# Optimization experiments

Hardware: AMD Instinct MI355X
Metric: run time of the kernel (lower is better)

Reference implementation:

```python
import jax, jax.numpy as jnp
import numpy as np

N = 50000      # nodes
E = 800000     # edges
H = 128        # num_node_hidden_channels
G = 50         # num_edge_gaussians
F = 128        # num_node_interaction_channels (= num_filters = out dim)
S = 2          # num_state_features
B = 256        # num graphs
NCONV = 2
CUTOFF = 5.0


def _ssp(x):
    # ShiftedSoftplus: softplus(x) - log(2)
    return jax.nn.softplus(x) - jnp.log(2.0).astype(x.dtype)


def _xavier(k, shape):
    fan_in = shape[-1]
    return (jax.random.normal(k, shape) / np.sqrt(fan_in)).astype(jnp.float32)


def setup_inputs() -> dict:
    key = jax.random.key(0)
    ks = jax.random.split(key, 16)
    h = jax.random.normal(ks[0], (N, H), dtype=jnp.float32)
    edge_index = jax.random.randint(ks[1], (2, E), 0, N, dtype=jnp.int64)
    edge_weight = jax.random.uniform(ks[2], (E,), dtype=jnp.float32) * CUTOFF
    edge_attr = jax.random.normal(ks[3], (E, G), dtype=jnp.float32)
    batch = jnp.sort(jax.random.randint(ks[4], (N,), 0, B, dtype=jnp.int64))
    state_attr = jax.random.normal(ks[5], (B, S), dtype=jnp.float32)
    # parameters, stacked over n_conv layers
    params = dict(
        lin1_w=_xavier(ks[6], (NCONV, H, H + S)),
        lin1_b=jnp.zeros((NCONV, H), jnp.float32),
        mlp_w1=_xavier(ks[7], (NCONV, F, G)),
        mlp_b1=jnp.zeros((NCONV, F), jnp.float32),
        mlp_w2=_xavier(ks[8], (NCONV, F, F)),
        mlp_b2=jnp.zeros((NCONV, F), jnp.float32),
        conv_lin1_w=_xavier(ks[9], (NCONV, F, H)),
        conv_lin2_w=_xavier(ks[10], (NCONV, H, F)),
        conv_lin2_b=jnp.zeros((NCONV, H), jnp.float32),
        out_w=_xavier(ks[11], (F, H)),
        out_b=jnp.zeros((F,), jnp.float32),
    )
    return dict(h=h, edge_weight=edge_weight, edge_attr=edge_attr,
                state_attr=state_attr, **params,
                edge_index=edge_index, batch=batch)


def _forward(h, edge_weight, edge_attr, state_attr,
             lin1_w, lin1_b, mlp_w1, mlp_b1, mlp_w2, mlp_b2,
             conv_lin1_w, conv_lin2_w, conv_lin2_b, out_w, out_b,
             edge_index, batch):
    src, dst = edge_index[0], edge_index[1]   # x_j gathered from src, aggregated at dst
    nB = state_attr.shape[0]
    # cosine cutoff envelope (same for all layers)
    C = 0.5 * (jnp.cos(edge_weight * (np.pi / CUTOFF)) + 1.0)   # [E]
    counts = jax.ops.segment_sum(jnp.ones((h.shape[0],), h.dtype), batch,
                                 num_segments=nB)               # [B]
    inv_counts = 1.0 / jnp.maximum(counts, 1.0)
    for i in range(NCONV):
        sa = state_attr[batch]                                  # [N,S]
        hs = jnp.concatenate([sa, h], axis=1)                   # [N,S+H]
        h2 = hs @ lin1_w[i].T + lin1_b[i]                       # [N,H]
        # edge filter MLP * cutoff
        eh = _ssp(edge_attr @ mlp_w1[i].T + mlp_b1[i]) @ mlp_w2[i].T + mlp_b2[i]
        W = eh * C[:, None]                                     # [E,F]
        # CFConv: lift -> gather-multiply -> scatter-add
        xf = h2 @ conv_lin1_w[i].T                              # [N,F]
        msg = xf[src] * W                                       # [E,F]
        agg = jax.ops.segment_sum(msg, dst, num_segments=h.shape[0])  # [N,F]
        xc = agg @ conv_lin2_w[i].T + conv_lin2_b[i]            # [N,H]
        h = h2 + _ssp(xc)                                       # residual + act
        # segment mean pooling over graphs, then global state update
        r = jax.ops.segment_sum(h, batch, num_segments=nB) * inv_counts[:, None]
        state_attr = jnp.broadcast_to(jnp.sum(r, axis=1, keepdims=True),
                                      state_attr.shape)
    return h @ out_w.T + out_b                                  # [N,F]


def reference(h, edge_weight, edge_attr, state_attr,
              lin1_w, lin1_b, mlp_w1, mlp_b1, mlp_w2, mlp_b2,
              conv_lin1_w, conv_lin2_w, conv_lin2_b, out_w, out_b,
              edge_index, batch):
    return _forward(h, edge_weight, edge_attr, state_attr,
                    lin1_w, lin1_b, mlp_w1, mlp_b1, mlp_w2, mlp_b2,
                    conv_lin1_w, conv_lin2_w, conv_lin2_b, out_w, out_b,
                    edge_index, batch)
```

## Files before the change

kernel.cpp:

```cpp
#include <hip/hip_runtime.h>

#define NN 50000
#define EE 800000
#define HH 128
#define GG 50
#define FF 128
#define SS 2
#define BB 256
#define SLOTW 8

typedef short bf16x8 __attribute__((ext_vector_type(8)));
typedef float floatx4 __attribute__((ext_vector_type(4)));

union FragU { bf16x8 v; unsigned short u[8]; unsigned int d[4]; uint4 q; };

__device__ __forceinline__ float bf2f(unsigned short u) {
    union { unsigned int i; float f; } c; c.i = ((unsigned int)u) << 16; return c.f;
}
__device__ __forceinline__ unsigned short f2bf(float f) {
    union { float f; unsigned int i; } c; c.f = f;
    unsigned int i = c.i;
    unsigned int r = (i + 0x7fffu + ((i >> 16) & 1u)) >> 16;
    return (unsigned short)r;
}
__device__ __forceinline__ float sspf(float x) {
    float l = __logf(1.f + __expf(x));
    l = (x > 20.f) ? x : l;
    return l - 0.69314718056f;
}
__device__ __forceinline__ bf16x8 f8frag(const float* p) {
    FragU f;
#pragma unroll
    for (int j = 0; j < 8; j++) f.u[j] = f2bf(p[j]);
    return f.v;
}
__device__ __forceinline__ bf16x8 load16(const unsigned short* p) {
    FragU f; f.q = *(const uint4*)p; return f.v;
}
__device__ __forceinline__ bf16x8 loaddw(const unsigned short* p) {
    FragU f; const unsigned int* pp = (const unsigned int*)p;
#pragma unroll
    for (int t = 0; t < 4; t++) f.d[t] = pp[t];
    return f.v;
}
__device__ __forceinline__ int clampi(int v, int hi) {
    v = (v < 0) ? 0 : v;
    return (v > hi) ? hi : v;
}

__global__ __launch_bounds__(256) void kConv(const float* __restrict__ s,
                                             unsigned short* __restrict__ d, int n) {
    for (int i = blockIdx.x * 256 + threadIdx.x; i < n; i += gridDim.x * 256)
        d[i] = f2bf(s[i]);
}

__global__ __launch_bounds__(256) void kConvW(const float* __restrict__ a0,
                                              const float* __restrict__ a1,
                                              const float* __restrict__ a2,
                                              const float* __restrict__ a3,
                                              const float* __restrict__ a4,
                                              const float* __restrict__ a5,
                                              unsigned short* __restrict__ d) {
    int i = blockIdx.x * 256 + threadIdx.x;
    float v;
    if (i < 12800)        v = a0[i];
    else if (i < 45568)   v = a1[i - 12800];
    else if (i < 78336)   v = a2[i - 45568];
    else if (i < 111104)  v = a3[i - 78336];
    else if (i < 144384)  v = a4[i - 111104];
    else if (i < 160768)  v = a5[i - 144384];
    else {
        int j = i - 160768;
        int k = j & 63;
        int nl = j >> 6;
        v = (k < 50) ? a0[nl * 50 + k] : 0.f;
    }
    d[i] = f2bf(v);
}

__global__ __launch_bounds__(256) void kPrep(const int* __restrict__ batch,
                                             int* __restrict__ counts,
                                             const float* __restrict__ sa_in,
                                             float* __restrict__ stateBuf) {
    int i = blockIdx.x * 256 + threadIdx.x;
    if (i < NN) atomicAdd(&counts[clampi(batch[i], BB - 1)], 1);
    if (i < BB * SS) stateBuf[i] = sa_in[i];
}

__global__ __launch_bounds__(256) void kHist(const int* __restrict__ eidx,
                                             int* __restrict__ cnt) {
    for (int e = blockIdx.x * 256 + threadIdx.x; e < EE; e += gridDim.x * 256)
        atomicAdd(&cnt[clampi(eidx[EE + e], NN - 1)], 1);
}

__global__ __launch_bounds__(1024) void kScanA(const int* __restrict__ cnt,
                                               int* __restrict__ off,
                                               int* __restrict__ blkSum) {
    __shared__ int s[1024];
    int tid = threadIdx.x;
    int g = blockIdx.x * 1024 + tid;
    int v = (g < NN) ? cnt[g] : 0;
    s[tid] = v;
    __syncthreads();
#pragma unroll
    for (int o = 1; o < 1024; o <<= 1) {
        int x = (tid >= o) ? s[tid - o] : 0;
        __syncthreads();
        s[tid] += x;
        __syncthreads();
    }
    if (g < NN) off[g] = s[tid] - v;
    if (tid == 1023) blkSum[blockIdx.x] = s[1023];
}
__global__ void kScanB(int* __restrict__ blkSum, int nb) {
    if (threadIdx.x == 0) {
        int acc = 0;
        for (int i = 0; i < nb; i++) { int t = blkSum[i]; blkSum[i] = acc; acc += t; }
    }
}
__global__ __launch_bounds__(256) void kScanC(int* __restrict__ off,
                                              const int* __restrict__ blkSum) {
    int g = blockIdx.x * 256 + threadIdx.x;
    if (g < NN) off[g] += blkSum[g >> 10];
}

__global__ __launch_bounds__(256) void kScatter(const int* __restrict__ eidx,
                                                const float* __restrict__ ew,
                                                const int* __restrict__ off,
                                                int* __restrict__ cur,
                                                int* __restrict__ pos,
                                                int* __restrict__ ePerm,
                                                int* __restrict__ dstS,
                                                int* __restrict__ srcS,
                                                float* __restrict__ cS) {
    for (int e = blockIdx.x * 256 + threadIdx.x; e < EE; e += gridDim.x * 256) {
        int d = clampi(eidx[EE + e], NN - 1);
        int p = off[d] + atomicAdd(&cur[d], 1);
        pos[e] = p;
        ePerm[p] = e;
        dstS[p] = d;
        srcS[p] = clampi(eidx[e], NN - 1);
        float w = ew[e];
        cS[p] = 0.5f * (__cosf(w * 0.62831853072f) + 1.f);
    }
}

__global__ __launch_bounds__(256) void kPermEA(const float* __restrict__ ea,
                                               const int* __restrict__ pos,
                                               unsigned short* __restrict__ eaSb) {
    int idx = blockIdx.x * 256 + threadIdx.x;
    int e = idx >> 2, part = idx & 3;
    int p = pos[e];
    const float* src = ea + (size_t)e * 50 + part * 16;
    FragU f0, f1;
#pragma unroll
    for (int j = 0; j < 8; j++) f0.u[j] = (part * 16 + j < 50) ? f2bf(src[j]) : 0;
#pragma unroll
    for (int j = 0; j < 8; j++) f1.u[j] = (part * 16 + 8 + j < 50) ? f2bf(src[8 + j]) : 0;
    uint4* d = (uint4*)(eaSb + (size_t)p * 64 + part * 16);
    d[0] = f0.q; d[1] = f1.q;
}

__global__ __launch_bounds__(256) void kA(const unsigned short* __restrict__ hb,
                                          const unsigned short* __restrict__ l1wb,
                                          const float* __restrict__ lin1w,
                                          const float* __restrict__ lin1b,
                                          const unsigned short* __restrict__ c1wb,
                                          const float* __restrict__ stateBuf,
                                          const int* __restrict__ batch,
                                          unsigned short* __restrict__ h2b,
                                          unsigned short* __restrict__ xfb) {
    __shared__ __align__(16) unsigned short P[64][136];
    int lane = threadIdx.x & 63;
    int wave = threadIdx.x >> 6;
    int m = lane & 15, q = lane >> 4;
    int rowBase = blockIdx.x * 64 + wave * 16;
    int arow = rowBase + m;
    int arowc = (arow < NN) ? arow : (NN - 1);

    floatx4 acc[8];
#pragma unroll
    for (int t = 0; t < 8; t++) acc[t] = (floatx4){0.f, 0.f, 0.f, 0.f};

#pragma unroll
    for (int k0 = 0; k0 < 128; k0 += 32) {
        bf16x8 a = load16(hb + (size_t)arowc * 128 + k0 + q * 8);
#pragma unroll
        for (int t = 0; t < 8; t++) {
            int n = t * 16 + m;
            bf16x8 b = loaddw(l1wb + (size_t)n * 130 + 2 + k0 + q * 8);
            acc[t] = __builtin_amdgcn_mfma_f32_16x16x32_bf16(a, b, acc[t], 0, 0, 0);
        }
    }

    int r0 = rowBase + q * 4;
    float s0[4], s1[4];
#pragma unroll
    for (int j = 0; j < 4; j++) {
        int r = r0 + j; int rc = (r < NN) ? r : (NN - 1);
        int g = clampi(batch[rc], BB - 1);
        s0[j] = stateBuf[g * 2 + 0];
        s1[j] = stateBuf[g * 2 + 1];
    }
#pragma unroll
    for (int t = 0; t < 8; t++) {
        int c = t * 16 + m;
        float w0 = lin1w[(size_t)c * 130 + 0];
        float w1 = lin1w[(size_t)c * 130 + 1];
        float bb = lin1b[c];
#pragma unroll
        for (int j = 0; j < 4; j++) {
            int r = r0 + j;
            unsigned short vb = f2bf(acc[t][j] + bb + s0[j] * w0 + s1[j] * w1);
            if (r < NN) h2b[(size_t)r * 128 + c] = vb;
            P[wave * 16 + q * 4 + j][c] = vb;
        }
    }
    __syncthreads();

    floatx4 acc2[8];
#pragma unroll
    for (int t = 0; t < 8; t++) acc2[t] = (floatx4){0.f, 0.f, 0.f, 0.f};
#pragma unroll
    for (int k0 = 0; k0 < 128; k0 += 32) {
        FragU fa; fa.q = *(const uint4*)&P[wave * 16 + m][k0 + q * 8];
#pragma unroll
        for (int t = 0; t < 8; t++) {
            int n = t * 16 + m;
            bf16x8 b = load16(c1wb + (size_t)n * 128 + k0 + q * 8);
            acc2[t] = __builtin_amdgcn_mfma_f32_16x16x32_bf16(fa.v, b, acc2[t], 0, 0, 0);
        }
    }
#pragma unroll
    for (int t = 0; t < 8; t++) {
        int c = t * 16 + m;
#pragma unroll
        for (int j = 0; j < 4; j++) {
            int r = r0 + j;
            if (r < NN) xfb[(size_t)r * 128 + c] = f2bf(acc2[t][j]);
        }
    }
}

__global__ __launch_bounds__(256) void kF(const unsigned short* __restrict__ eaSb,
                                          const unsigned short* __restrict__ w1pb,
                                          const float* __restrict__ b1,
                                          const unsigned short* __restrict__ w2b,
                                          const float* __restrict__ b2,
                                          const int* __restrict__ dstS,
                                          const int* __restrict__ srcS,
                                          const float* __restrict__ cS,
                                          const unsigned short* __restrict__ xfb,
                                          float* __restrict__ agg) {
    __shared__ __align__(16) unsigned short P[4][16][136];
    __shared__ float accW[4][SLOTW][132];
    __shared__ int slotDst[4][16];

    int tid = threadIdx.x;
    int lane = tid & 63;
    int w = tid >> 6;
    int m = lane & 15, q = lane >> 4;
    int base = (blockIdx.x * 4 + w) * 16;

    int gr = lane >> 2, gc = lane & 3;
    int gsrc = srcS[base + gr];
    const uint4* gs = (const uint4*)&xfb[(size_t)gsrc * 128 + gc * 32];
    uint4 x0 = gs[0], x1 = gs[1], x2 = gs[2], x3 = gs[3];

    int eRow = base + m;
    bf16x8 a0 = load16(eaSb + (size_t)eRow * 64 + 0  + q * 8);
    bf16x8 a1 = load16(eaSb + (size_t)eRow * 64 + 32 + q * 8);

    int d_r = dstS[base + m];
    int dp = __shfl(d_r, (lane - 1) & 63);
    bool flag = (m == 0) || (d_r != dp);
    unsigned long long bm = __ballot(flag ? 1 : 0);
    unsigned int bmlow = (unsigned int)(bm & 0xFFFFull);
    int D = __popc(bmlow);
    int Dc = (D < SLOTW) ? D : SLOTW;
    {
        int slot_m = __popc(bmlow & ((2u << m) - 1u)) - 1;
        if (lane < 16 && flag) slotDst[w][slot_m] = d_r;
    }
    float Cj[4]; int sl[4];
#pragma unroll
    for (int j = 0; j < 4; j++) {
        int r = q * 4 + j;
        Cj[j] = cS[base + r];
        sl[j] = __popc(bmlow & ((2u << r) - 1u)) - 1;
    }

    {
        float* fl = &accW[w][0][0];
        for (int i = lane; i < Dc * 132; i += 64) fl[i] = 0.f;
    }

    floatx4 acc[8];
#pragma unroll
    for (int t = 0; t < 8; t++) acc[t] = (floatx4){0.f, 0.f, 0.f, 0.f};
#pragma unroll
    for (int t = 0; t < 8; t++) {
        int n = t * 16 + m;
        bf16x8 b = load16(w1pb + (size_t)n * 64 + 0 + q * 8);
        acc[t] = __builtin_amdgcn_mfma_f32_16x16x32_bf16(a0, b, acc[t], 0, 0, 0);
    }
#pragma unroll
    for (int t = 0; t < 8; t++) {
        int n = t * 16 + m;
        bf16x8 b = load16(w1pb + (size_t)n * 64 + 32 + q * 8);
        acc[t] = __builtin_amdgcn_mfma_f32_16x16x32_bf16(a1, b, acc[t], 0, 0, 0);
    }
#pragma unroll
    for (int t = 0; t < 8; t++) {
        int c = t * 16 + m;
        float bb = b1[c];
#pragma unroll
        for (int j = 0; j < 4; j++)
            P[w][q * 4 + j][c] = f2bf(sspf(acc[t][j] + bb));
    }

    floatx4 acc2[8];
#pragma unroll
    for (int t = 0; t < 8; t++) acc2[t] = (floatx4){0.f, 0.f, 0.f, 0.f};
#pragma unroll
    for (int k0 = 0; k0 < 128; k0 += 32) {
        FragU fa; fa.q = *(const uint4*)&P[w][m][k0 + q * 8];
#pragma unroll
        for (int t = 0; t < 8; t++) {
            int n = t * 16 + m;
            bf16x8 b = load16(w2b + (size_t)n * 128 + k0 + q * 8);
            acc2[t] = __builtin_amdgcn_mfma_f32_16x16x32_bf16(fa.v, b, acc2[t], 0, 0, 0);
        }
    }

    {
        uint4* dptr = (uint4*)&P[w][gr][gc * 32];
        dptr[0] = x0; dptr[1] = x1; dptr[2] = x2; dptr[3] = x3;
    }

#pragma unroll
    for (int t = 0; t < 8; t++) {
        int c = t * 16 + m;
        float bb = b2[c];
        float v4[4];
#pragma unroll
        for (int j = 0; j < 4; j++)
            v4[j] = (acc2[t][j] + bb) * Cj[j] * bf2f(P[w][q * 4 + j][c]);
        float run = v4[0];
#pragma unroll
        for (int j = 1; j < 4; j++) {
            if (sl[j] == sl[j - 1]) run += v4[j];
            else {
                int s = sl[j - 1];
                if (s < SLOTW) atomicAdd(&accW[w][s][c], run);
                else unsafeAtomicAdd(&agg[(size_t)slotDst[w][s] * 128 + c], run);
                run = v4[j];
            }
        }
        {
            int s = sl[3];
            if (s < SLOTW) atomicAdd(&accW[w][s][c], run);
            else unsafeAtomicAdd(&agg[(size_t)slotDst[w][s] * 128 + c], run);
        }
    }

    for (int i = lane; i < Dc * 128; i += 64) {
        int s = i >> 7, cc = i & 127;
        float v = accW[w][s][cc];
        size_t o = (size_t)slotDst[w][s] * 128 + cc;
        if (s > 0 && s < D - 1) agg[o] = v;
        else unsafeAtomicAdd(&agg[o], v);
    }
}

__global__ __launch_bounds__(256) void kE2(const float* __restrict__ ea,
                                           const unsigned short* __restrict__ w1b,
                                           const float* __restrict__ b1,
                                           const unsigned short* __restrict__ w2b,
                                           const float* __restrict__ b2,
                                           const int* __restrict__ ePerm,
                                           const int* __restrict__ dstS,
                                           const int* __restrict__ srcS,
                                           const float* __restrict__ cS,
                                           const unsigned short* __restrict__ xfb,
                                           float* __restrict__ agg) {
    __shared__ __align__(16) unsigned short P[64][136];
    __shared__ float accS[64][132];
    __shared__ int sSlot[64];
    __shared__ int sSlotDst[64];
    __shared__ int sD;

    int tid = threadIdx.x;
    int lane = tid & 63;
    int wave = tid >> 6;
    int m = lane & 15, q = lane >> 4;
    int base = blockIdx.x * 64;

    float* accFlat = &accS[0][0];
    for (int i = tid; i < 64 * 132; i += 256) accFlat[i] = 0.f;

    if (tid < 64) {
        int i = tid;
        int di = dstS[base + i];
        bool flag = (i == 0) || (di != dstS[base + i - 1]);
        unsigned long long bm = __ballot(flag ? 1 : 0);
        unsigned long long low = (i == 63) ? ~0ull : ((1ull << (i + 1)) - 1ull);
        int slot = (int)__popcll(bm & low) - 1;
        sSlot[i] = slot;
        if (flag) sSlotDst[slot] = di;
        if (i == 63) sD = slot + 1;
    }

    int eRow = ePerm[base + wave * 16 + m];

    floatx4 acc[8];
#pragma unroll
    for (int t = 0; t < 8; t++) acc[t] = (floatx4){0.f, 0.f, 0.f, 0.f};
    {
        bf16x8 a = f8frag(ea + (size_t)eRow * 50 + q * 8);
#pragma unroll
        for (int t = 0; t < 8; t++) {
            int n = t * 16 + m;
            bf16x8 b = loaddw(w1b + (size_t)n * 50 + q * 8);
            acc[t] = __builtin_amdgcn_mfma_f32_16x16x32_bf16(a, b, acc[t], 0, 0, 0);
        }
    }
    {
        int kbase = 32 + q * 8;
        FragU fa;
        const float* pa = ea + (size_t)eRow * 50 + kbase;
#pragma unroll
        for (int j = 0; j < 8; j++) fa.u[j] = (kbase + j < 50) ? f2bf(pa[j]) : 0;
#pragma unroll
        for (int t = 0; t < 8; t++) {
            int n = t * 16 + m;
            FragU fb;
            const unsigned int* pb = (const unsigned int*)(w1b + (size_t)n * 50 + kbase);
#pragma unroll
            for (int t2 = 0; t2 < 4; t2++) fb.d[t2] = (kbase + 2 * t2 < 50) ? pb[t2] : 0u;
            acc[t] = __builtin_amdgcn_mfma_f32_16x16x32_bf16(fa.v, fb.v, acc[t], 0, 0, 0);
        }
    }
#pragma unroll
    for (int t = 0; t < 8; t++) {
        int c = t * 16 + m;
        float bb = b1[c];
#pragma unroll
        for (int j = 0; j < 4; j++)
            P[wave * 16 + q * 4 + j][c] = f2bf(sspf(acc[t][j] + bb));
    }
    __syncthreads();

    floatx4 acc2[8];
#pragma unroll
    for (int t = 0; t < 8; t++) acc2[t] = (floatx4){0.f, 0.f, 0.f, 0.f};
#pragma unroll
    for (int k0 = 0; k0 < 128; k0 += 32) {
        FragU fa; fa.q = *(const uint4*)&P[wave * 16 + m][k0 + q * 8];
#pragma unroll
        for (int t = 0; t < 8; t++) {
            int n = t * 16 + m;
            bf16x8 b = load16(w2b + (size_t)n * 128 + k0 + q * 8);
            acc2[t] = __builtin_amdgcn_mfma_f32_16x16x32_bf16(fa.v, b, acc2[t], 0, 0, 0);
        }
    }

    int sl[4], srcj[4]; float Cj[4];
#pragma unroll
    for (int j = 0; j < 4; j++) {
        int r = wave * 16 + q * 4 + j;
        int g = base + r;
        sl[j] = sSlot[r];
        Cj[j] = cS[g];
        srcj[j] = srcS[g];
    }
#pragma unroll
    for (int t = 0; t < 8; t++) {
        int c = t * 16 + m;
        float bb = b2[c];
        float v4[4];
#pragma unroll
        for (int j = 0; j < 4; j++)
            v4[j] = (acc2[t][j] + bb) * Cj[j] * bf2f(xfb[(size_t)srcj[j] * 128 + c]);
        float run = v4[0];
#pragma unroll
        for (int j = 1; j < 4; j++) {
            if (sl[j] == sl[j - 1]) run += v4[j];
            else { atomicAdd(&accS[sl[j - 1]][c], run); run = v4[j]; }
        }
        atomicAdd(&accS[sl[3]][c], run);
    }
    __syncthreads();

    int D = sD;
    for (int idx = tid; idx < D * 128; idx += 256) {
        int s = idx >> 7, c = idx & 127;
        unsafeAtomicAdd(&agg[(size_t)sSlotDst[s] * 128 + c], accS[s][c]);
    }
}

__global__ __launch_bounds__(256) void kC(const float* __restrict__ agg,
                                          const unsigned short* __restrict__ wb,
                                          const float* __restrict__ b,
                                          const unsigned short* __restrict__ h2b,
                                          unsigned short* __restrict__ hnb,
                                          const int* __restrict__ batch,
                                          float* __restrict__ pool,
                                          int doPool) {
    int lane = threadIdx.x & 63;
    int wave = threadIdx.x >> 6;
    int m = lane & 15, q = lane >> 4;
    int rowBase = blockIdx.x * 64 + wave * 16;
    int arow = rowBase + m;
    int arowc = (arow < NN) ? arow : (NN - 1);

    floatx4 acc[8];
#pragma unroll
    for (int t = 0; t < 8; t++) acc[t] = (floatx4){0.f, 0.f, 0.f, 0.f};

#pragma unroll
    for (int k0 = 0; k0 < 128; k0 += 32) {
        bf16x8 fa = f8frag(agg + (size_t)arowc * 128 + k0 + q * 8);
#pragma unroll
        for (int t = 0; t < 8; t++) {
            int n = t * 16 + m;
            bf16x8 bfr = load16(wb + (size_t)n * 128 + k0 + q * 8);
            acc[t] = __builtin_amdgcn_mfma_f32_16x16x32_bf16(fa, bfr, acc[t], 0, 0, 0);
        }
    }

    int r0 = rowBase + q * 4;
    float vsum[4] = {0.f, 0.f, 0.f, 0.f};
#pragma unroll
    for (int t = 0; t < 8; t++) {
        int c = t * 16 + m;
        float bb = b[c];
#pragma unroll
        for (int j = 0; j < 4; j++) {
            int r = r0 + j; int rc = (r < NN) ? r : (NN - 1);
            float v = bf2f(h2b[(size_t)rc * 128 + c]) + sspf(acc[t][j] + bb);
            if (r < NN) {
                hnb[(size_t)r * 128 + c] = f2bf(v);
                vsum[j] += v;
            }
        }
    }
    if (doPool) {
#pragma unroll
        for (int j = 0; j < 4; j++) {
            float v = vsum[j];
#pragma unroll
            for (int off = 1; off < 16; off <<= 1) v += __shfl_xor(v, off, 16);
            int r = r0 + j;
            if (m == 0 && r < NN) unsafeAtomicAdd(&pool[clampi(batch[r], BB - 1)], v);
        }
    }
}

__global__ __launch_bounds__(256) void kS(const float* __restrict__ pool,
                                          const int* __restrict__ counts,
                                          float* __restrict__ stateBuf) {
    int b = threadIdx.x;
    if (b < BB) {
        float c = (float)counts[b];
        c = (c < 1.f) ? 1.f : c;
        float v = pool[b] / c;
        stateBuf[b * 2 + 0] = v;
        stateBuf[b * 2 + 1] = v;
    }
}

__global__ __launch_bounds__(256) void kOut(const unsigned short* __restrict__ hnb,
                                            const unsigned short* __restrict__ owb,
                                            const float* __restrict__ ob,
                                            float* __restrict__ out) {
    int lane = threadIdx.x & 63;
    int wave = threadIdx.x >> 6;
    int m = lane & 15, q = lane >> 4;
    int rowBase = blockIdx.x * 64 + wave * 16;
    int arow = rowBase + m;
    int arowc = (arow < NN) ? arow : (NN - 1);

    floatx4 acc[8];
#pragma unroll
    for (int t = 0; t < 8; t++) acc[t] = (floatx4){0.f, 0.f, 0.f, 0.f};
#pragma unroll
    for (int k0 = 0; k0 < 128; k0 += 32) {
        bf16x8 a = load16(hnb + (size_t)arowc * 128 + k0 + q * 8);
#pragma unroll
        for (int t = 0; t < 8; t++) {
            int n = t * 16 + m;
            bf16x8 bfr = load16(owb + (size_t)n * 128 + k0 + q * 8);
            acc[t] = __builtin_amdgcn_mfma_f32_16x16x32_bf16(a, bfr, acc[t], 0, 0, 0);
        }
    }
    int r0 = rowBase + q * 4;
#pragma unroll
    for (int t = 0; t < 8; t++) {
        int c = t * 16 + m;
        float bb = ob[c];
#pragma unroll
        for (int j = 0; j < 4; j++) {
            int r = r0 + j;
            if (r < NN) out[(size_t)r * 128 + c] = acc[t][j] + bb;
        }
    }
}

extern "C" void kernel_launch(void* const* d_in, const int* in_sizes, int n_in,
                              void* d_out, int out_size, void* d_ws, size_t ws_size,
                              hipStream_t stream) {
    const float* h     = (const float*)d_in[0];
    const float* ew    = (const float*)d_in[1];
    const float* ea    = (const float*)d_in[2];
    const float* sa    = (const float*)d_in[3];
    const float* lin1w = (const float*)d_in[4];
    const float* lin1b = (const float*)d_in[5];
    const float* mw1   = (const float*)d_in[6];
    const float* mb1   = (const float*)d_in[7];
    const float* mw2   = (const float*)d_in[8];
    const float* mb2   = (const float*)d_in[9];
    const float* c1w   = (const float*)d_in[10];
    const float* c2w   = (const float*)d_in[11];
    const float* c2b   = (const float*)d_in[12];
    const float* outw  = (const float*)d_in[13];
    const float* outb  = (const float*)d_in[14];
    const int* eidx    = (const int*)d_in[15];
    const int* batch   = (const int*)d_in[16];
    float* out = (float*)d_out;

    char* ws = (char*)d_ws;
    unsigned short* hnb   = (unsigned short*)(ws);
    unsigned short* h2b   = (unsigned short*)(ws + 12800000);
    unsigned short* xfb   = (unsigned short*)(ws + 25600000);
    float*          agg   = (float*)(ws + 38400000);
    int*            pos   = (int*)(ws + 64000000);
    int*            ePerm = (int*)(ws + 67200000);
    int*            dstS  = (int*)(ws + 70400000);
    int*            srcS  = (int*)(ws + 73600000);
    float*          cS    = (float*)(ws + 76800000);
    int*            cnt   = (int*)(ws + 80000000);
    int*            off   = (int*)(ws + 80200000);
    int*            cur   = (int*)(ws + 80400000);
    int*            blkSum= (int*)(ws + 80600000);
    unsigned short* wb    = (unsigned short*)(ws + 80600512);
    float*          pool  = (float*)(ws + 80954816);
    int*            counts= (int*)(ws + 80955840);
    float*          stateBuf = (float*)(ws + 80956864);
    const size_t EAOFF = 80958912;
    unsigned short* eaSb = (unsigned short*)(ws + EAOFF);

    const size_t need = EAOFF + (size_t)EE * 64 * 2;
    const int useF = (ws_size >= need) ? 1 : 0;

    unsigned short* mw1b = wb;
    unsigned short* mw2b = wb + 12800;
    unsigned short* c1wb = wb + 45568;
    unsigned short* c2wb = wb + 78336;
    unsigned short* l1wb = wb + 111104;
    unsigned short* owb  = wb + 144384;
    unsigned short* w1pb = wb + 160768;

    hipMemsetAsync(cnt, 0, NN * 4, stream);
    hipMemsetAsync(cur, 0, NN * 4, stream);
    hipMemsetAsync(counts, 0, BB * 4, stream);
    hipMemsetAsync(pool, 0, BB * 4, stream);

    kPrep<<<(NN + 255) / 256, 256, 0, stream>>>(batch, counts, sa, stateBuf);
    kHist<<<1024, 256, 0, stream>>>(eidx, cnt);
    kScanA<<<(NN + 1023) / 1024, 1024, 0, stream>>>(cnt, off, blkSum);
    kScanB<<<1, 64, 0, stream>>>(blkSum, (NN + 1023) / 1024);
    kScanC<<<(NN + 255) / 256, 256, 0, stream>>>(off, blkSum);
    kScatter<<<1024, 256, 0, stream>>>(eidx, ew, off, cur, pos, ePerm, dstS, srcS, cS);

    kConvW<<<177152 / 256, 256, 0, stream>>>(mw1, mw2, c1w, c2w, lin1w, outw, wb);
    kConv<<<4096, 256, 0, stream>>>(h, hnb, NN * 128);
    if (useF) {
        kPermEA<<<(EE * 4) / 256, 256, 0, stream>>>(ea, pos, eaSb);
    }

    const int gridN = (NN + 63) / 64;
    const int gridE = EE / 64;

    for (int i = 0; i < 2; i++) {
        hipMemsetAsync(agg, 0, (size_t)NN * 128 * 4, stream);
        kA<<<gridN, 256, 0, stream>>>(hnb,
                                      l1wb + (size_t)i * 128 * 130,
                                      lin1w + (size_t)i * 128 * 130,
                                      lin1b + (size_t)i * 128,
                                      c1wb + (size_t)i * 128 * 128,
                                      stateBuf, batch, h2b, xfb);
        if (useF) {
            kF<<<gridE, 256, 0, stream>>>(eaSb,
                                          w1pb + (size_t)i * 128 * 64,
                                          mb1 + (size_t)i * 128,
                                          mw2b + (size_t)i * 128 * 128,
                                          mb2 + (size_t)i * 128,
                                          dstS, srcS, cS, xfb, agg);
        } else {
            kE2<<<gridE, 256, 0, stream>>>(ea,
                                           mw1b + (size_t)i * 128 * 50,
                                           mb1 + (size_t)i * 128,
                                           mw2b + (size_t)i * 128 * 128,
                                           mb2 + (size_t)i * 128,
                                           ePerm, dstS, srcS, cS, xfb, agg);
        }
        kC<<<gridN, 256, 0, stream>>>(agg,
                                      c2wb + (size_t)i * 128 * 128,
                                      c2b + (size_t)i * 128,
                                      h2b, hnb, batch, pool, (i == 0) ? 1 : 0);
        if (i == 0) kS<<<1, 256, 0, stream>>>(pool, counts, stateBuf);
    }
    kOut<<<gridN, 256, 0, stream>>>(hnb, owb, outb, out);
}
```

Before: 1.556 ms.

## Make edge-filter kernel persistent with LDS-cached W2 and register-held W1

kF now launches a fixed grid of 500 blocks. Each wave processes 25 consecutive 16-edge tiles instead of one. The mlp_w2 weights are staged once per block into swizzled LDS, and the W1 fragments and biases are kept in registers, which removes repeated global or L2 weight loads for every tile. The next tile's edge attributes are prefetched while the current one computes. The shared-memory slot count drops from 8 to 4. Costs are higher LDS and register use, which may lower occupancy, and fewer blocks to hide gather latency.

```diff
diff --git a/kernel.cpp b/kernel.cpp
--- a/kernel.cpp
+++ b/kernel.cpp
@@ -7,7 +7,9 @@
 #define FF 128
 #define SS 2
 #define BB 256
-#define SLOTW 8
+#define SLOTW 4
+#define KFBLK 500
+#define NTPW 25
 
 typedef short bf16x8 __attribute__((ext_vector_type(8)));
 typedef float floatx4 __attribute__((ext_vector_type(4)));
@@ -252,6 +254,7 @@
                                           const float* __restrict__ cS,
                                           const unsigned short* __restrict__ xfb,
                                           float* __restrict__ agg) {
+    __shared__ __align__(16) char w2L[32768];
     __shared__ __align__(16) unsigned short P[4][16][136];
     __shared__ float accW[4][SLOTW][132];
     __shared__ int slotDst[4][16];
@@ -260,116 +263,138 @@
     int lane = tid & 63;
     int w = tid >> 6;
     int m = lane & 15, q = lane >> 4;
-    int base = (blockIdx.x * 4 + w) * 16;
-
-    int gr = lane >> 2, gc = lane & 3;
-    int gsrc = srcS[base + gr];
-    const uint4* gs = (const uint4*)&xfb[(size_t)gsrc * 128 + gc * 32];
-    uint4 x0 = gs[0], x1 = gs[1], x2 = gs[2], x3 = gs[3];
-
-    int eRow = base + m;
-    bf16x8 a0 = load16(eaSb + (size_t)eRow * 64 + 0  + q * 8);
-    bf16x8 a1 = load16(eaSb + (size_t)eRow * 64 + 32 + q * 8);
-
-    int d_r = dstS[base + m];
-    int dp = __shfl(d_r, (lane - 1) & 63);
-    bool flag = (m == 0) || (d_r != dp);
-    unsigned long long bm = __ballot(flag ? 1 : 0);
-    unsigned int bmlow = (unsigned int)(bm & 0xFFFFull);
-    int D = __popc(bmlow);
-    int Dc = (D < SLOTW) ? D : SLOTW;
-    {
-        int slot_m = __popc(bmlow & ((2u << m) - 1u)) - 1;
-        if (lane < 16 && flag) slotDst[w][slot_m] = d_r;
-    }
-    float Cj[4]; int sl[4];
-#pragma unroll
-    for (int j = 0; j < 4; j++) {
-        int r = q * 4 + j;
-        Cj[j] = cS[base + r];
-        sl[j] = __popc(bmlow & ((2u << r) - 1u)) - 1;
-    }
-
-    {
-        float* fl = &accW[w][0][0];
-        for (int i = lane; i < Dc * 132; i += 64) fl[i] = 0.f;
-    }
-
-    floatx4 acc[8];
-#pragma unroll
-    for (int t = 0; t < 8; t++) acc[t] = (floatx4){0.f, 0.f, 0.f, 0.f};
+
+    for (int idx = tid; idx < 128 * 16; idx += 256) {
+        int n = idx >> 4, ch = idx & 15;
+        uint4 v = *(const uint4*)(w2b + (size_t)n * 128 + ch * 8);
+        int bo = n * 256 + ((ch * 16) ^ ((n & 7) << 4));
+        *(uint4*)(w2L + bo) = v;
+    }
+
+    bf16x8 w1lo[8], w1hi[8];
+    float b1v[8], b2v[8];
 #pragma unroll
     for (int t = 0; t < 8; t++) {
         int n = t * 16 + m;
-        bf16x8 b = load16(w1pb + (size_t)n * 64 + 0 + q * 8);
-        acc[t] = __builtin_amdgcn_mfma_f32_16x16x32_bf16(a0, b, acc[t], 0, 0, 0);
-    }
-#pragma unroll
-    for (int t = 0; t < 8; t++) {
-        int n = t * 16 + m;
-        bf16x8 b = load16(w1pb + (size_t)n * 64 + 32 + q * 8);
-        acc[t] = __builtin_amdgcn_mfma_f32_16x16x32_bf16(a1, b, acc[t], 0, 0, 0);
-    }
-#pragma unroll
-    for (int t = 0; t < 8; t++) {
-        int c = t * 16 + m;
-        float bb = b1[c];
+        w1lo[t] = load16(w1pb + (size_t)n * 64 + q * 8);
+        w1hi[t] = load16(w1pb + (size_t)n * 64 + 32 + q * 8);
+        b1v[t] = b1[n];
+        b2v[t] = b2[n];
+    }
+    __syncthreads();
+
+    int base = (blockIdx.x * 4 + w) * (NTPW * 16);
+    int gr = lane >> 2, gc = lane & 3;
+
+    bf16x8 a0 = load16(eaSb + (size_t)(base + m) * 64 + q * 8);
+    bf16x8 a1 = load16(eaSb + (size_t)(base + m) * 64 + 32 + q * 8);
+
+    for (int it = 0; it < NTPW; ++it, base += 16) {
+        bf16x8 a0n = a0, a1n = a1;
+        if (it < NTPW - 1) {
+            a0n = load16(eaSb + (size_t)(base + 16 + m) * 64 + q * 8);
+            a1n = load16(eaSb + (size_t)(base + 16 + m) * 64 + 32 + q * 8);
+        }
+        int d_r = dstS[base + m];
+        int gsrc = srcS[base + gr];
+        float Cj[4];
+#pragma unroll
+        for (int j = 0; j < 4; j++) Cj[j] = cS[base + q * 4 + j];
+
+        floatx4 acc[8];
+#pragma unroll
+        for (int t = 0; t < 8; t++) {
+            floatx4 z = (floatx4){0.f, 0.f, 0.f, 0.f};
+            z = __builtin_amdgcn_mfma_f32_16x16x32_bf16(a0, w1lo[t], z, 0, 0, 0);
+            acc[t] = __builtin_amdgcn_mfma_f32_16x16x32_bf16(a1, w1hi[t], z, 0, 0, 0);
+        }
+
+        int dp = __shfl(d_r, (lane - 1) & 63);
+        bool flag = (m == 0) || (d_r != dp);
+        unsigned long long bm = __ballot(flag ? 1 : 0);
+        unsigned int bmlow = (unsigned int)(bm & 0xFFFFull);
+        int D = __popc(bmlow);
+        int Dc = (D < SLOTW) ? D : SLOTW;
+        {
+            int slot_m = __popc(bmlow & ((2u << m) - 1u)) - 1;
+            if (lane < 16 && flag) slotDst[w][slot_m] = d_r;
+        }
+        int sl[4];
 #pragma unroll
         for (int j = 0; j < 4; j++)
-            P[w][q * 4 + j][c] = f2bf(sspf(acc[t][j] + bb));
-    }
-
-    floatx4 acc2[8];
-#pragma unroll
-    for (int t = 0; t < 8; t++) acc2[t] = (floatx4){0.f, 0.f, 0.f, 0.f};
-#pragma unroll
-    for (int k0 = 0; k0 < 128; k0 += 32) {
-        FragU fa; fa.q = *(const uint4*)&P[w][m][k0 + q * 8];
-#pragma unroll
-        for (int t = 0; t < 8; t++) {
-            int n = t * 16 + m;
-            bf16x8 b = load16(w2b + (size_t)n * 128 + k0 + q * 8);
-            acc2[t] = __builtin_amdgcn_mfma_f32_16x16x32_bf16(fa.v, b, acc2[t], 0, 0, 0);
-        }
-    }
-
-    {
-        uint4* dptr = (uint4*)&P[w][gr][gc * 32];
-        dptr[0] = x0; dptr[1] = x1; dptr[2] = x2; dptr[3] = x3;
-    }
-
-#pragma unroll
-    for (int t = 0; t < 8; t++) {
-        int c = t * 16 + m;
-        float bb = b2[c];
-        float v4[4];
-#pragma unroll
-        for (int j = 0; j < 4; j++)
-            v4[j] = (acc2[t][j] + bb) * Cj[j] * bf2f(P[w][q * 4 + j][c]);
-        float run = v4[0];
-#pragma unroll
-        for (int j = 1; j < 4; j++) {
-            if (sl[j] == sl[j - 1]) run += v4[j];
-            else {
-                int s = sl[j - 1];
+            sl[j] = __popc(bmlow & ((2u << (q * 4 + j)) - 1u)) - 1;
+
+#pragma unroll
+        for (int t = 0; t < 8; t++) {
+            int c = t * 16 + m;
+#pragma unroll
+            for (int j = 0; j < 4; j++)
+                P[w][q * 4 + j][c] = f2bf(sspf(acc[t][j] + b1v[t]));
+        }
+
+        const uint4* gs = (const uint4*)&xfb[(size_t)gsrc * 128 + gc * 32];
+        uint4 x0 = gs[0], x1 = gs[1], x2 = gs[2], x3 = gs[3];
+
+        {
+            float* fl = &accW[w][0][0];
+            for (int i = lane; i < Dc * 132; i += 64) fl[i] = 0.f;
+        }
+
+        floatx4 acc2[8];
+#pragma unroll
+        for (int t = 0; t < 8; t++) acc2[t] = (floatx4){0.f, 0.f, 0.f, 0.f};
+#pragma unroll
+        for (int k0 = 0; k0 < 128; k0 += 32) {
+            FragU fa; fa.q = *(const uint4*)&P[w][m][k0 + q * 8];
+#pragma unroll
+            for (int t = 0; t < 8; t++) {
+                int n = t * 16 + m;
+                int bo = n * 256 + ((((k0 + q * 8) * 2)) ^ ((n & 7) << 4));
+                bf16x8 b = load16((const unsigned short*)(w2L + bo));
+                acc2[t] = __builtin_amdgcn_mfma_f32_16x16x32_bf16(fa.v, b, acc2[t], 0, 0, 0);
+            }
+        }
+
+        {
+            uint4* dptr = (uint4*)&P[w][gr][gc * 32];
+            dptr[0] = x0; dptr[1] = x1; dptr[2] = x2; dptr[3] = x3;
+        }
+
+#pragma unroll
+        for (int t = 0; t < 8; t++) {
+            int c = t * 16 + m;
+            float bb = b2v[t];
+            float v4[4];
+#pragma unroll
+            for (int j = 0; j < 4; j++)
+                v4[j] = (acc2[t][j] + bb) * Cj[j] * bf2f(P[w][q * 4 + j][c]);
+            float run = v4[0];
+#pragma unroll
+            for (int j = 1; j < 4; j++) {
+                if (sl[j] == sl[j - 1]) run += v4[j];
+                else {
+                    int s = sl[j - 1];
+                    if (s < SLOTW) atomicAdd(&accW[w][s][c], run);
+                    else unsafeAtomicAdd(&agg[(size_t)slotDst[w][s] * 128 + c], run);
+                    run = v4[j];
+                }
+            }
+            {
+                int s = sl[3];
                 if (s < SLOTW) atomicAdd(&accW[w][s][c], run);
                 else unsafeAtomicAdd(&agg[(size_t)slotDst[w][s] * 128 + c], run);
-                run = v4[j];
             }
         }
-        {
-            int s = sl[3];
-            if (s < SLOTW) atomicAdd(&accW[w][s][c], run);
-            else unsafeAtomicAdd(&agg[(size_t)slotDst[w][s] * 128 + c], run);
-        }
-    }
-
-    for (int i = lane; i < Dc * 128; i += 64) {
-        int s = i >> 7, cc = i & 127;
-        float v = accW[w][s][cc];
-        size_t o = (size_t)slotDst[w][s] * 128 + cc;
-        if (s > 0 && s < D - 1) agg[o] = v;
-        else unsafeAtomicAdd(&agg[o], v);
+
+        for (int i = lane; i < Dc * 128; i += 64) {
+            int s = i >> 7, cc = i & 127;
+            float v = accW[w][s][cc];
+            size_t o = (size_t)slotDst[w][s] * 128 + cc;
+            if (s > 0 && s < D - 1) agg[o] = v;
+            else unsafeAtomicAdd(&agg[o], v);
+        }
+
+        a0 = a0n; a1 = a1n;
     }
 }
 
@@ -680,7 +705,6 @@
     }
 
     const int gridN = (NN + 63) / 64;
-    const int gridE = EE / 64;
 
     for (int i = 0; i < 2; i++) {
         hipMemsetAsync(agg, 0, (size_t)NN * 128 * 4, stream);
@@ -691,19 +715,19 @@
                                       c1wb + (size_t)i * 128 * 128,
                                       stateBuf, batch, h2b, xfb);
         if (useF) {
-            kF<<<gridE, 256, 0, stream>>>(eaSb,
+            kF<<<KFBLK, 256, 0, stream>>>(eaSb,
                                           w1pb + (size_t)i * 128 * 64,
                                           mb1 + (size_t)i * 128,
                                           mw2b + (size_t)i * 128 * 128,
                                           mb2 + (size_t)i * 128,
                                           dstS, srcS, cS, xfb, agg);
         } else {
-            kE2<<<gridE, 256, 0, stream>>>(ea,
-                                           mw1b + (size_t)i * 128 * 50,
-                                           mb1 + (size_t)i * 128,
-                                           mw2b + (size_t)i * 128 * 128,
-                                           mb2 + (size_t)i * 128,
-                                           ePerm, dstS, srcS, cS, xfb, agg);
+            kE2<<<EE / 64, 256, 0, stream>>>(ea,
+                                             mw1b + (size_t)i * 128 * 50,
+                                             mb1 + (size_t)i * 128,
+                                             mw2b + (size_t)i * 128 * 128,
+                                             mb2 + (size_t)i * 128,
+                                             ePerm, dstS, srcS, cS, xfb, agg);
         }
         kC<<<gridN, 256, 0, stream>>>(agg,
                                       c2wb + (size_t)i * 128 * 128,
```

New measurement: 1.289 ms. 1.21x faster.
